# Optimization experiments

Measured on AMD Instinct MI355X. Metric: run time of the kernel, lower is better.

The kernel has to match this reference:

```python
import jax, jax.numpy as jnp
import numpy as np

N_NODES = 100000
N_EDGES = 1000000
D_FEAT = 64
N_FILTER = 64
N_CLASSES = 16


def gcn_norm(edge_idx, n):
    """Add self-loops and compute symmetric normalization D^-1/2 (A+I) D^-1/2."""
    loop = jnp.arange(n, dtype=edge_idx.dtype)
    src = jnp.concatenate([edge_idx[0], loop])  # [E+N]
    dst = jnp.concatenate([edge_idx[1], loop])  # [E+N]
    w = jnp.ones(src.shape[0], dtype=jnp.float32)
    deg = jax.ops.segment_sum(w, dst, num_segments=n)  # in-degree incl. self-loop
    dinv = jnp.where(deg > 0, jax.lax.rsqrt(deg), 0.0)
    norm = dinv[src] * w * dinv[dst]  # [E+N]
    return src, dst, norm


def gcn_conv(x, W, b, src, dst, norm, n):
    h = x @ W                                   # [n, f] dense transform first (f <= d)
    msg = h[src] * norm[:, None]                # gather + scale  [E+N, f]
    out = jax.ops.segment_sum(msg, dst, num_segments=n)  # scatter-add  [n, f]
    return out + b


def setup_inputs() -> dict:
    key = jax.random.key(0)
    k1, k2, k3, k4 = jax.random.split(key, 4)
    X = jax.random.normal(k1, (N_NODES, D_FEAT), dtype=jnp.float32)
    edge_idx = jax.random.randint(k2, (2, N_EDGES), 0, N_NODES, dtype=jnp.int64)
    W1 = jax.random.normal(k3, (D_FEAT, N_FILTER), dtype=jnp.float32) * 0.05
    b1 = jnp.zeros((N_FILTER,), dtype=jnp.float32)
    W2 = jax.random.normal(k4, (N_FILTER, N_CLASSES), dtype=jnp.float32) * 0.05
    b2 = jnp.zeros((N_CLASSES,), dtype=jnp.float32)
    return {"X": X, "edge_idx": edge_idx, "W1": W1, "b1": b1, "W2": W2, "b2": b2}


def reference(X, edge_idx, W1, b1, W2, b2):
    n = X.shape[0]
    src, dst, norm = gcn_norm(edge_idx, n)
    x = gcn_conv(X, W1, b1, src, dst, norm, n)
    x = jax.nn.relu(x)
    # dropout p=0 -> identity
    x = gcn_conv(x, W2, b2, src, dst, norm, n)
    return x  # raw logits; pred_layer is not applied in the torch forward
```

## Files before the change

kernel.cpp:

```cpp
#include <hip/hip_runtime.h>
#include <hip/hip_bf16.h>


constexpr int N = 100000;
constexpr int E = 1000000;
constexpr int NB = (N + 511) / 512;
constexpr int CAP = 6144;
constexpr int CSTRIDE = 32;
constexpr int CHUNK = 4096;
constexpr int NBLK = (E + CHUNK - 1) / CHUNK;
constexpr int NPW = 13;
constexpr int NW = (N + NPW - 1) / NPW;
constexpr int NWBLK = (NW + 3) / 4;

__device__ __forceinline__ float rl_f(float v, int l) {
    return __int_as_float(__builtin_amdgcn_readlane(__float_as_int(v), l));
}
__device__ __forceinline__ float bflo(unsigned u) { return __uint_as_float(u << 16); }
__device__ __forceinline__ float bfhi(unsigned u) { return __uint_as_float(u & 0xffff0000u); }

__global__ void k_bfill(const int* __restrict__ src, const int* __restrict__ dst,
                        int* __restrict__ cursor, int* __restrict__ bkt) {
    __shared__ int hist[256];
    __shared__ int lbase[256];
    __shared__ int gbase[256];
    __shared__ int lcur[256];
    __shared__ int stage[CHUNK];
    __shared__ unsigned char sbkt[CHUNK];
    int t = threadIdx.x;
    int e0 = blockIdx.x * CHUNK;
    int cnt = min(CHUNK, E - e0);

    hist[t] = 0;
    __syncthreads();
    for (int j = t; j < cnt; j += 256)
        atomicAdd(&hist[dst[e0 + j] >> 9], 1);
    __syncthreads();
    int h = hist[t];
    lbase[t] = h;
    __syncthreads();
    for (int off = 1; off < 256; off <<= 1) {
        int x = (t >= off) ? lbase[t - off] : 0;
        __syncthreads();
        lbase[t] += x;
        __syncthreads();
    }
    int excl = lbase[t] - h;
    __syncthreads();
    lbase[t] = excl;
    lcur[t] = 0;
    if (t < NB) gbase[t] = h ? atomicAdd(&cursor[t * CSTRIDE], h) : 0;
    __syncthreads();
    for (int j = t; j < cnt; j += 256) {
        int d = dst[e0 + j];
        int b = d >> 9;
        int pos = lbase[b] + atomicAdd(&lcur[b], 1);
        stage[pos] = ((d & 511) << 17) | src[e0 + j];
        sbkt[pos] = (unsigned char)b;
    }
    __syncthreads();
    for (int j = t; j < cnt; j += 256) {
        int b = sbkt[j];
        int gpos = gbase[b] + (j - lbase[b]);
        if (gpos < CAP) bkt[b * CAP + gpos] = stage[j];
    }
}

__global__ void k_bfine(const int* __restrict__ cursor, const int* __restrict__ bkt,
                        int* __restrict__ row_ptr, float* __restrict__ dinv,
                        int* __restrict__ csr_src) {
    __shared__ int sd[256];
    __shared__ int cnt[512];
    __shared__ int excl[512];
    __shared__ int s2[256];
    int b = blockIdx.x;
    int t = threadIdx.x;
    int c = (t < NB) ? cursor[t * CSTRIDE] : 0;
    sd[t] = c;
    __syncthreads();
    for (int off = 1; off < 256; off <<= 1) {
        int x = (t >= off) ? sd[t - off] : 0;
        __syncthreads();
        sd[t] += x;
        __syncthreads();
    }
    int m = cursor[b * CSTRIDE];
    int base = sd[b] - m;
    if (b == 0 && t == 0) row_ptr[N] = E;
    const int* bb = bkt + b * CAP;
    cnt[t] = 0; cnt[t + 256] = 0;
    __syncthreads();
    for (int j = t; j < m; j += 256) atomicAdd(&cnt[bb[j] >> 17], 1);
    __syncthreads();
    int pairSum = cnt[2 * t] + cnt[2 * t + 1];
    s2[t] = pairSum;
    __syncthreads();
    for (int off = 1; off < 256; off <<= 1) {
        int x = (t >= off) ? s2[t - off] : 0;
        __syncthreads();
        s2[t] += x;
        __syncthreads();
    }
    int exclPair = s2[t] - pairSum;
    excl[2 * t] = exclPair;
    excl[2 * t + 1] = exclPair + cnt[2 * t];
    __syncthreads();
#pragma unroll
    for (int hh = 0; hh < 2; ++hh) {
        int k = t + hh * 256;
        int node = b * 512 + k;
        if (node < N) {
            row_ptr[node] = base + excl[k];
            dinv[node] = rsqrtf((float)(cnt[k] + 1));
        }
    }
    __syncthreads();
    for (int j = t; j < m; j += 256) {
        int v = bb[j];
        int p = atomicAdd(&excl[v >> 17], 1);
        csr_src[base + p] = v & 0x1FFFF;
    }
}

__global__ void k_gemm1(const float* __restrict__ X, const float* __restrict__ W1,
                        const float* __restrict__ dinv, __hip_bfloat16* __restrict__ h1s,
                        __hip_bfloat16* __restrict__ h2s) {
    int t = threadIdx.x;
    int lane = t & 63;
    int wid = (blockIdx.x * 256 + t) >> 6;
    if (blockIdx.x == 0) {
        if (t < 64) h1s[(size_t)N * 64 + t] = __float2bfloat16(0.f);
        if (t < 16) h2s[(size_t)N * 16 + t] = __float2bfloat16(0.f);
    }
    float w1[64];
#pragma unroll
    for (int k = 0; k < 64; ++k) w1[k] = W1[k * 64 + lane];
    for (int row = wid; row < N; row += 4096) {
        float x = X[(size_t)row * 64 + lane];
        float acc = 0.f;
#pragma unroll
        for (int k = 0; k < 64; ++k) acc = fmaf(rl_f(x, k), w1[k], acc);
        acc *= dinv[row];
        float up = __shfl_xor(acc, 1);
        if (!(lane & 1)) {
            __hip_bfloat162 p;
            p.x = __float2bfloat16(acc);
            p.y = __float2bfloat16(up);
            *(__hip_bfloat162*)(h1s + (size_t)row * 64 + lane) = p;
        }
    }
}

__global__ void k_layer12(const int* __restrict__ row_ptr, const int* __restrict__ csr_src,
                          const float* __restrict__ dinv, const __hip_bfloat16* __restrict__ h1s,
                          const float* __restrict__ b1, const float* __restrict__ W2,
                          __hip_bfloat16* __restrict__ h2s) {
    __shared__ float sy[4][8][72];
    int t = threadIdx.x;
    int lane = t & 63;
    int w = t >> 6;
    int g8 = lane >> 3;
    int qo = (lane & 7) << 4;
    int g16 = lane >> 4, c16 = lane & 15;
    int wid = blockIdx.x * 4 + w;
    int d0 = wid * NPW;
    if (d0 >= N) return;
    int dend = min(d0 + NPW, N);
    float w2[16];
#pragma unroll
    for (int j = 0; j < 16; ++j) w2[j] = W2[(g16 * 16 + j) * 16 + c16];
    float b1v = b1[lane];
    const char* Hb = (const char*)h1s;

    int rp0 = row_ptr[d0];
    for (int d = d0; d < dend; ++d) {
        int rp1 = row_ptr[d + 1];
        float dv = dinv[d];
        float a[8] = {0, 0, 0, 0, 0, 0, 0, 0};
        if (g8 == 0) {
            uint4 u = *(const uint4*)(Hb + (((unsigned)d << 7) | qo));
            a[0] = bflo(u.x); a[1] = bfhi(u.x); a[2] = bflo(u.y); a[3] = bfhi(u.y);
            a[4] = bflo(u.z); a[5] = bfhi(u.z); a[6] = bflo(u.w); a[7] = bfhi(u.w);
        }
        for (int base = rp0; base < rp1; base += 64) {
            int nloc = min(64, rp1 - base);
            int sidx = (lane < nloc) ? csr_src[base + lane] : N;
            int steps = (nloc + 7) >> 3;
            for (int j = 0; j < steps; ++j) {
                int s = __shfl(sidx, (j << 3) | g8);
                uint4 u = *(const uint4*)(Hb + (((unsigned)s << 7) | qo));
                a[0] += bflo(u.x); a[1] += bfhi(u.x);
                a[2] += bflo(u.y); a[3] += bfhi(u.y);
                a[4] += bflo(u.z); a[5] += bfhi(u.z);
                a[6] += bflo(u.w); a[7] += bfhi(u.w);
            }
        }
        rp0 = rp1;
        float* row = &sy[w][g8][(lane & 7) << 3];
        *(float4*)row = make_float4(a[0], a[1], a[2], a[3]);
        *(float4*)(row + 4) = make_float4(a[4], a[5], a[6], a[7]);
        __builtin_amdgcn_s_waitcnt(0);
        float ysum = sy[w][0][lane] + sy[w][1][lane] + sy[w][2][lane] + sy[w][3][lane]
                   + sy[w][4][lane] + sy[w][5][lane] + sy[w][6][lane] + sy[w][7][lane];
        float y = fmaxf(fmaf(dv, ysum, b1v), 0.f);
        float o = 0.f;
#pragma unroll
        for (int j = 0; j < 16; ++j) o = fmaf(__shfl(y, (lane & 48) | j), w2[j], o);
        o += __shfl_xor(o, 16);
        o += __shfl_xor(o, 32);
        o *= dv;
        float oup = __shfl_xor(o, 1);
        if (lane < 16 && !(lane & 1)) {
            __hip_bfloat162 p;
            p.x = __float2bfloat16(o);
            p.y = __float2bfloat16(oup);
            *(__hip_bfloat162*)(h2s + (size_t)d * 16 + lane) = p;
        }
    }
}

__global__ void k_gather2(const int* __restrict__ row_ptr, const int* __restrict__ csr_src,
                          const float* __restrict__ dinv, const __hip_bfloat16* __restrict__ h2s,
                          const float* __restrict__ b2, float* __restrict__ out) {
    int t = threadIdx.x;
    int lane = t & 63;
    int g4 = lane >> 2;
    int q2 = lane & 3;
    int qo = q2 << 3;
    int wid = blockIdx.x * 4 + (t >> 6);
    int d0 = wid * NPW;
    if (d0 >= N) return;
    int dend = min(d0 + NPW, N);
    float b2v[4];
#pragma unroll
    for (int k = 0; k < 4; ++k) b2v[k] = b2[q2 * 4 + k];
    const char* Hb = (const char*)h2s;

    int rp0 = row_ptr[d0];
    for (int d = d0; d < dend; ++d) {
        int rp1 = row_ptr[d + 1];
        float dv = dinv[d];
        float a[4] = {0, 0, 0, 0};
        if (g4 == 0) {
            uint2 u = *(const uint2*)(Hb + (((unsigned)d << 5) | qo));
            a[0] = bflo(u.x); a[1] = bfhi(u.x); a[2] = bflo(u.y); a[3] = bfhi(u.y);
        }
        for (int base = rp0; base < rp1; base += 64) {
            int nloc = min(64, rp1 - base);
            int sidx = (lane < nloc) ? csr_src[base + lane] : N;
            int steps = (nloc + 15) >> 4;
            for (int j = 0; j < steps; ++j) {
                int s = __shfl(sidx, (j << 4) | g4);
                uint2 u = *(const uint2*)(Hb + (((unsigned)s << 5) | qo));
                a[0] += bflo(u.x); a[1] += bfhi(u.x);
                a[2] += bflo(u.y); a[3] += bfhi(u.y);
            }
        }
        rp0 = rp1;
#pragma unroll
        for (int k = 0; k < 4; ++k) {
            a[k] += __shfl_xor(a[k], 4);
            a[k] += __shfl_xor(a[k], 8);
            a[k] += __shfl_xor(a[k], 16);
            a[k] += __shfl_xor(a[k], 32);
        }
        if (lane < 4) {
            float4 r;
            r.x = fmaf(dv, a[0], b2v[0]);
            r.y = fmaf(dv, a[1], b2v[1]);
            r.z = fmaf(dv, a[2], b2v[2]);
            r.w = fmaf(dv, a[3], b2v[3]);
            *(float4*)(out + (size_t)d * 16 + q2 * 4) = r;
        }
    }
}

extern "C" void kernel_launch(void* const* d_in, const int* in_sizes, int n_in,
                              void* d_out, int out_size, void* d_ws, size_t ws_size,
                              hipStream_t stream) {
    const float* X  = (const float*)d_in[0];
    const int*   ei = (const int*)d_in[1];
    const float* W1 = (const float*)d_in[2];
    const float* b1 = (const float*)d_in[3];
    const float* W2 = (const float*)d_in[4];
    const float* b2 = (const float*)d_in[5];
    float* out = (float*)d_out;

    int* cursor  = (int*)d_ws;
    int* row_ptr = cursor + NB * CSTRIDE;
    int* bkt     = row_ptr + N + 4;
    int* csr_src = bkt + NB * CAP;
    float* dinv  = (float*)(csr_src + E);
    __hip_bfloat16* h1s = (__hip_bfloat16*)(dinv + N);
    __hip_bfloat16* h2s = h1s + (size_t)(N + 1) * 64;

    const int* src = ei;
    const int* dst = ei + E;

    hipMemsetAsync(cursor, 0, NB * CSTRIDE * sizeof(int), stream);
    k_bfill<<<NBLK, 256, 0, stream>>>(src, dst, cursor, bkt);
    k_bfine<<<NB, 256, 0, stream>>>(cursor, bkt, row_ptr, dinv, csr_src);
    k_gemm1<<<1024, 256, 0, stream>>>(X, W1, dinv, h1s, h2s);
    k_layer12<<<NWBLK, 256, 0, stream>>>(row_ptr, csr_src, dinv, h1s, b1, W2, h2s);
    k_gather2<<<NWBLK, 256, 0, stream>>>(row_ptr, csr_src, dinv, h2s, b2, out);
}
```

Before: 213.9 us.

## Vectorize CSR bucket reads, stage GEMM1 rows in LDS, unroll gathers, shrink NPW

The CSR build kernel now reads bucket entries as int4 vectors, with a scalar tail loop. GEMM1 stages four X rows per wave in shared memory instead of broadcasting values through readlane. The layer-1 gather issues two independent 16-byte loads per step, padding partial batches with the zero sentinel row, so more memory requests are in flight. Nodes per wave drop from 13 to 6 for finer load balance, at the cost of more waves and more W2 reloads. The int4 cast assumes 16-byte aligned bucket bases, and GEMM1 has no bounds guard for row groups past N (N is a multiple of 4, so this holds here).

Result: faster. 194.2 us (median of 2 runs) (-9.2%).

```diff
diff --git a/kernel.cpp b/kernel.cpp
--- a/kernel.cpp
+++ b/kernel.cpp
@@ -9,13 +9,10 @@
 constexpr int CSTRIDE = 32;
 constexpr int CHUNK = 4096;
 constexpr int NBLK = (E + CHUNK - 1) / CHUNK;
-constexpr int NPW = 13;
+constexpr int NPW = 6;
 constexpr int NW = (N + NPW - 1) / NPW;
 constexpr int NWBLK = (NW + 3) / 4;
 
-__device__ __forceinline__ float rl_f(float v, int l) {
-    return __int_as_float(__builtin_amdgcn_readlane(__float_as_int(v), l));
-}
 __device__ __forceinline__ float bflo(unsigned u) { return __uint_as_float(u << 16); }
 __device__ __forceinline__ float bfhi(unsigned u) { return __uint_as_float(u & 0xffff0000u); }
 
@@ -88,9 +85,16 @@
     int base = sd[b] - m;
     if (b == 0 && t == 0) row_ptr[N] = E;
     const int* bb = bkt + b * CAP;
+    const int4* bb4 = (const int4*)bb;
+    int m4 = m >> 2;
     cnt[t] = 0; cnt[t + 256] = 0;
     __syncthreads();
-    for (int j = t; j < m; j += 256) atomicAdd(&cnt[bb[j] >> 17], 1);
+    for (int j = t; j < m4; j += 256) {
+        int4 v = bb4[j];
+        atomicAdd(&cnt[v.x >> 17], 1); atomicAdd(&cnt[v.y >> 17], 1);
+        atomicAdd(&cnt[v.z >> 17], 1); atomicAdd(&cnt[v.w >> 17], 1);
+    }
+    for (int j = (m4 << 2) + t; j < m; j += 256) atomicAdd(&cnt[bb[j] >> 17], 1);
     __syncthreads();
     int pairSum = cnt[2 * t] + cnt[2 * t + 1];
     s2[t] = pairSum;
@@ -115,7 +119,14 @@
         }
     }
     __syncthreads();
-    for (int j = t; j < m; j += 256) {
+    for (int j = t; j < m4; j += 256) {
+        int4 v = bb4[j];
+        int p0 = atomicAdd(&excl[v.x >> 17], 1); csr_src[base + p0] = v.x & 0x1FFFF;
+        int p1 = atomicAdd(&excl[v.y >> 17], 1); csr_src[base + p1] = v.y & 0x1FFFF;
+        int p2 = atomicAdd(&excl[v.z >> 17], 1); csr_src[base + p2] = v.z & 0x1FFFF;
+        int p3 = atomicAdd(&excl[v.w >> 17], 1); csr_src[base + p3] = v.w & 0x1FFFF;
+    }
+    for (int j = (m4 << 2) + t; j < m; j += 256) {
         int v = bb[j];
         int p = atomicAdd(&excl[v >> 17], 1);
         csr_src[base + p] = v & 0x1FFFF;
@@ -125,8 +136,10 @@
 __global__ void k_gemm1(const float* __restrict__ X, const float* __restrict__ W1,
                         const float* __restrict__ dinv, __hip_bfloat16* __restrict__ h1s,
                         __hip_bfloat16* __restrict__ h2s) {
+    __shared__ float sX[4][4][64];
     int t = threadIdx.x;
     int lane = t & 63;
+    int w = t >> 6;
     int wid = (blockIdx.x * 256 + t) >> 6;
     if (blockIdx.x == 0) {
         if (t < 64) h1s[(size_t)N * 64 + t] = __float2bfloat16(0.f);
@@ -135,18 +148,23 @@
     float w1[64];
 #pragma unroll
     for (int k = 0; k < 64; ++k) w1[k] = W1[k * 64 + lane];
-    for (int row = wid; row < N; row += 4096) {
-        float x = X[(size_t)row * 64 + lane];
-        float acc = 0.f;
-#pragma unroll
-        for (int k = 0; k < 64; ++k) acc = fmaf(rl_f(x, k), w1[k], acc);
-        acc *= dinv[row];
-        float up = __shfl_xor(acc, 1);
-        if (!(lane & 1)) {
-            __hip_bfloat162 p;
-            p.x = __float2bfloat16(acc);
-            p.y = __float2bfloat16(up);
-            *(__hip_bfloat162*)(h1s + (size_t)row * 64 + lane) = p;
+    for (int r4 = wid * 4; r4 < N; r4 += 4096 * 4) {
+#pragma unroll
+        for (int j = 0; j < 4; ++j) sX[w][j][lane] = X[(size_t)(r4 + j) * 64 + lane];
+        __builtin_amdgcn_s_waitcnt(0);
+#pragma unroll
+        for (int j = 0; j < 4; ++j) {
+            float acc = 0.f;
+#pragma unroll
+            for (int k = 0; k < 64; ++k) acc = fmaf(sX[w][j][k], w1[k], acc);
+            acc *= dinv[r4 + j];
+            float up = __shfl_xor(acc, 1);
+            if (!(lane & 1)) {
+                __hip_bfloat162 p;
+                p.x = __float2bfloat16(acc);
+                p.y = __float2bfloat16(up);
+                *(__hip_bfloat162*)(h1s + (size_t)(r4 + j) * 64 + lane) = p;
+            }
         }
     }
 }
@@ -185,14 +203,17 @@
         for (int base = rp0; base < rp1; base += 64) {
             int nloc = min(64, rp1 - base);
             int sidx = (lane < nloc) ? csr_src[base + lane] : N;
-            int steps = (nloc + 7) >> 3;
+            int steps = (nloc + 15) >> 4;
             for (int j = 0; j < steps; ++j) {
-                int s = __shfl(sidx, (j << 3) | g8);
-                uint4 u = *(const uint4*)(Hb + (((unsigned)s << 7) | qo));
-                a[0] += bflo(u.x); a[1] += bfhi(u.x);
-                a[2] += bflo(u.y); a[3] += bfhi(u.y);
-                a[4] += bflo(u.z); a[5] += bfhi(u.z);
-                a[6] += bflo(u.w); a[7] += bfhi(u.w);
+                int b0 = (j << 4) | g8;
+                int s0 = __shfl(sidx, b0);
+                int s1 = __shfl(sidx, b0 | 8);
+                uint4 u0 = *(const uint4*)(Hb + (((unsigned)s0 << 7) | qo));
+                uint4 u1 = *(const uint4*)(Hb + (((unsigned)s1 << 7) | qo));
+                a[0] += bflo(u0.x); a[1] += bfhi(u0.x); a[2] += bflo(u0.y); a[3] += bfhi(u0.y);
+                a[4] += bflo(u0.z); a[5] += bfhi(u0.z); a[6] += bflo(u0.w); a[7] += bfhi(u0.w);
+                a[0] += bflo(u1.x); a[1] += bfhi(u1.x); a[2] += bflo(u1.y); a[3] += bfhi(u1.y);
+                a[4] += bflo(u1.z); a[5] += bfhi(u1.z); a[6] += bflo(u1.w); a[7] += bfhi(u1.w);
             }
         }
         rp0 = rp1;
```
